# Performance work log

Hardware: AMD Instinct MI355X
Metric: run time of the kernel (lower is better)

The kernel has to match this reference:

```python
import jax, jax.numpy as jnp
import numpy as np

N_NODES = 100000


def _gcn_conv(h, row, col, norm, W, b):
    # h: [N, Fin] -> [N, Fout]; standard GCN: scatter-add of normalized
    # neighbor messages after linear transform.
    h = h @ W                                   # [N, Fout]
    msg = h[col] * norm[:, None]                # [E, Fout] gather + scale
    out = jax.ops.segment_sum(msg, row, num_segments=N_NODES)
    return out + b


def setup_inputs() -> dict:
    key = jax.random.key(0)
    k1, k2, k3, k4 = jax.random.split(key, 4)
    N, E, F_IN, HID, OUT = N_NODES, 3200000, 512, 16, 40
    x = jax.random.normal(k1, (N, F_IN), dtype=jnp.float32)
    edge_index = jax.random.randint(k2, (2, E), 0, N, dtype=jnp.int64)
    W1 = jax.random.normal(k3, (F_IN, HID), dtype=jnp.float32) * (1.0 / np.sqrt(F_IN))
    b1 = jnp.zeros((HID,), dtype=jnp.float32)
    W2 = jax.random.normal(k4, (HID, OUT), dtype=jnp.float32) * (1.0 / np.sqrt(HID))
    b2 = jnp.zeros((OUT,), dtype=jnp.float32)
    return {"x": x, "edge_index": edge_index, "W1": W1, "b1": b1, "W2": W2, "b2": b2}


def reference(x, edge_index, W1, b1, W2, b2):
    N = N_NODES
    # add self-loops (GCN convention)
    loop = jnp.arange(N, dtype=edge_index.dtype)
    row = jnp.concatenate([edge_index[0], loop])  # target nodes
    col = jnp.concatenate([edge_index[1], loop])  # source nodes
    # symmetric normalization deg^-1/2 * deg^-1/2
    deg = jax.ops.segment_sum(jnp.ones_like(row, dtype=x.dtype), row, num_segments=N)
    dinv = jnp.where(deg > 0, jax.lax.rsqrt(deg), 0.0)
    norm = dinv[row] * dinv[col]                  # [E+N]

    h = _gcn_conv(x, row, col, norm, W1, b1)
    h = jax.nn.relu(h)
    out = _gcn_conv(h, row, col, norm, W2, b2)
    return out
```

## Files before the change

### kernel.cpp

```cpp
#include <hip/hip_runtime.h>

#define N_NODES 100000
#define F_IN 512
#define HID 16
#define F_OUT 40

#define NB 784
#define BSHIFT 7
#define ROWS_PB 128
#define BCAP 4608
#define CUR_PAD 16
#define APAD 17
#define PARTB 512
#define SROW 129

__global__ void k_zero(int* __restrict__ g) {
    int i = blockIdx.x * 256 + threadIdx.x;
    if (i < NB * CUR_PAD) g[i] = 0;
}

__global__ __launch_bounds__(512) void k_fat(const float* __restrict__ x,
                                             const float* __restrict__ W1,
                                             const int* __restrict__ ei, int E,
                                             int* __restrict__ gcursor,
                                             unsigned int* __restrict__ sortbuf,
                                             float* __restrict__ Hs) {
    __shared__ float smem[8 * 64 * APAD];
    int t = threadIdx.x;
    if (blockIdx.x < PARTB) {
        int* lcnt = (int*)smem;
        int* gb   = lcnt + NB;
        int epb = (E + PARTB - 1) / PARTB;
        int base = blockIdx.x * epb;
        int lim = min(base + epb, E);
        for (int cbase = base; cbase < lim; cbase += 4096) {
            int cend = min(cbase + 4096, lim);
            for (int i = t; i < NB; i += 512) lcnt[i] = 0;
            __syncthreads();
            unsigned int v[8]; int bkt[8], mi[8];
#pragma unroll
            for (int i = 0; i < 8; ++i) {
                int e = cbase + i * 512 + t;
                bkt[i] = -1;
                if (e < cend) {
                    int r = ei[e], c = ei[E + e];
                    bkt[i] = r >> BSHIFT;
                    v[i] = ((unsigned)(r & (ROWS_PB - 1)) << 17) | (unsigned)c;
                    mi[i] = atomicAdd(&lcnt[bkt[i]], 1);
                }
            }
            __syncthreads();
            for (int i = t; i < NB; i += 512)
                gb[i] = atomicAdd(&gcursor[i * CUR_PAD], lcnt[i]);
            __syncthreads();
#pragma unroll
            for (int i = 0; i < 8; ++i)
                if (bkt[i] >= 0) {
                    int idx = gb[bkt[i]] + mi[i];
                    if (idx < BCAP) sortbuf[(size_t)bkt[i] * BCAP + idx] = v[i];
                }
            __syncthreads();
        }
    } else {
        int bid = blockIdx.x - PARTB;
        int tilebase = bid * 64;
        int srow = t >> 5;
        int sseg = t & 31;
        int crow = t & 63;
        int ksub = __builtin_amdgcn_readfirstlane(t >> 6);

        float acc[HID];
#pragma unroll
        for (int f = 0; f < HID; ++f) acc[f] = 0.0f;

        float4 rg[4];
#pragma unroll
        for (int q = 0; q < 4; ++q) {
            int r = tilebase + q * 16 + srow;
            r = min(r, N_NODES - 1);
            rg[q] = *reinterpret_cast<const float4*>(x + (size_t)r * F_IN + sseg * 4);
        }
        for (int s = 0; s < 4; ++s) {
            __syncthreads();
#pragma unroll
            for (int q = 0; q < 4; ++q) {
                int base = (q * 16 + srow) * SROW + sseg * 4;
                smem[base + 0] = rg[q].x;
                smem[base + 1] = rg[q].y;
                smem[base + 2] = rg[q].z;
                smem[base + 3] = rg[q].w;
            }
            __syncthreads();
            if (s < 3) {
#pragma unroll
                for (int q = 0; q < 4; ++q) {
                    int r = tilebase + q * 16 + srow;
                    r = min(r, N_NODES - 1);
                    rg[q] = *reinterpret_cast<const float4*>(
                        x + (size_t)r * F_IN + (s + 1) * 128 + sseg * 4);
                }
            }
            const float* wp = W1 + (s * 128 + ksub * 16) * HID;
            int lbase = crow * SROW + ksub * 16;
#pragma unroll
            for (int kk = 0; kk < 16; ++kk) {
                float xv = smem[lbase + kk];
#pragma unroll
                for (int f = 0; f < HID; ++f)
                    acc[f] = fmaf(xv, wp[kk * HID + f], acc[f]);
            }
        }
        __syncthreads();
        int rbase = (ksub * 64 + crow) * APAD;
#pragma unroll
        for (int f = 0; f < HID; ++f) smem[rbase + f] = acc[f];
        __syncthreads();
#pragma unroll
        for (int p = 0; p < 2; ++p) {
            int o = p * 512 + t;
            int r = o >> 4, f = o & 15;
            int rgl = tilebase + r;
            if (rgl < N_NODES) {
                float sum = 0.0f;
#pragma unroll
                for (int c = 0; c < 8; ++c) sum += smem[(c * 64 + r) * APAD + f];
                Hs[(size_t)rgl * HID + f] = sum;
            }
        }
    }
}

__global__ __launch_bounds__(256) void k_build(const unsigned int* __restrict__ sortbuf,
                                               const int* __restrict__ gcursor,
                                               int* __restrict__ rowptr,
                                               float* __restrict__ dinv,
                                               int* __restrict__ colv,
                                               float* __restrict__ Hs) {
    __shared__ int bb[NB];
    __shared__ int s[256];
    __shared__ int hist[ROWS_PB];
    __shared__ int rstart[ROWS_PB];
    __shared__ int cur[ROWS_PB];
    __shared__ float sdinv[ROWS_PB];
    int b = blockIdx.x, t = threadIdx.x;

    int l0 = 0, l1 = 0, l2 = 0, l3 = 0;
    if (t < 196) {
        l0 = min(gcursor[(t * 4 + 0) * CUR_PAD], BCAP);
        l1 = min(gcursor[(t * 4 + 1) * CUR_PAD], BCAP);
        l2 = min(gcursor[(t * 4 + 2) * CUR_PAD], BCAP);
        l3 = min(gcursor[(t * 4 + 3) * CUR_PAD], BCAP);
    }
    int part = l0 + l1 + l2 + l3;
    s[t] = part;
    __syncthreads();
    for (int off = 1; off < 256; off <<= 1) {
        int a = (t >= off) ? s[t - off] : 0;
        __syncthreads();
        s[t] += a;
        __syncthreads();
    }
    if (t < 196) {
        int ex = s[t] - part;
        bb[t * 4 + 0] = ex;
        bb[t * 4 + 1] = ex + l0;
        bb[t * 4 + 2] = ex + l0 + l1;
        bb[t * 4 + 3] = ex + l0 + l1 + l2;
    }
    if (t < ROWS_PB) hist[t] = 0;
    __syncthreads();
    int gbase = bb[b];
    int n = min(gcursor[b * CUR_PAD], BCAP);
    if (b == 0 && t == 0) rowptr[N_NODES] = s[255];

    const unsigned int* sb = sortbuf + (size_t)b * BCAP;
    for (int i = t; i < n; i += 256) atomicAdd(&hist[sb[i] >> 17], 1);
    __syncthreads();
    int c0 = (t < ROWS_PB) ? hist[t] : 0;
    s[t] = c0;
    __syncthreads();
    for (int off = 1; off < 256; off <<= 1) {
        int a = (t >= off) ? s[t - off] : 0;
        __syncthreads();
        s[t] += a;
        __syncthreads();
    }
    if (t < ROWS_PB) {
        int ex = s[t] - c0;
        rstart[t] = ex;
        cur[t] = 0;
        float dv = rsqrtf((float)(c0 + 1));
        sdinv[t] = dv;
        int g = b * ROWS_PB + t;
        if (g < N_NODES) {
            rowptr[g] = gbase + ex;
            dinv[g] = dv;
        }
    }
    __syncthreads();
    for (int i = t; i < n; i += 256) {
        unsigned int v = sb[i];
        int lr = v >> 17;
        int pos = atomicAdd(&cur[lr], 1);
        colv[gbase + rstart[lr] + pos] = (int)(v & 0x1FFFFu);
    }
    __syncthreads();
    for (int i = t; i < ROWS_PB * 4; i += 256) {
        int row = i >> 2, q = i & 3;
        int g = b * ROWS_PB + row;
        if (g < N_NODES) {
            float4* p = reinterpret_cast<float4*>(Hs + (size_t)g * HID + q * 4);
            float4 vv = *p;
            float dv = sdinv[row];
            vv.x *= dv; vv.y *= dv; vv.z *= dv; vv.w *= dv;
            *p = vv;
        }
    }
}

__global__ __launch_bounds__(256) void k_agg1(const int* __restrict__ rowptr,
                                              const int* __restrict__ colv,
                                              const float* __restrict__ dinv,
                                              const float* __restrict__ Hs,
                                              const float* __restrict__ b1,
                                              float* __restrict__ h1s) {
    int wid = __builtin_amdgcn_readfirstlane((blockIdx.x * 256 + threadIdx.x) >> 6);
    if (wid >= N_NODES) return;
    int lane = threadIdx.x & 63;
    int f4 = lane & 3, sub = lane >> 2;
    int beg = rowptr[wid], end = rowptr[wid + 1];
    float dr = dinv[wid];
    float4 acc = make_float4(0.f, 0.f, 0.f, 0.f);
    for (int j = beg + sub; j < end; j += 16) {
        int c = colv[j];
        float4 hv = *reinterpret_cast<const float4*>(Hs + (size_t)c * HID + f4 * 4);
        acc.x += hv.x; acc.y += hv.y; acc.z += hv.z; acc.w += hv.w;
    }
#pragma unroll
    for (int d = 4; d < 64; d <<= 1) {
        acc.x += __shfl_xor(acc.x, d);
        acc.y += __shfl_xor(acc.y, d);
        acc.z += __shfl_xor(acc.z, d);
        acc.w += __shfl_xor(acc.w, d);
    }
    if (sub == 0) {
        float4 self = *reinterpret_cast<const float4*>(Hs + (size_t)wid * HID + f4 * 4);
        float4 bb = *reinterpret_cast<const float4*>(b1 + f4 * 4);
        float4 o;
        o.x = fmaxf((acc.x + self.x) * dr + bb.x, 0.f) * dr;
        o.y = fmaxf((acc.y + self.y) * dr + bb.y, 0.f) * dr;
        o.z = fmaxf((acc.z + self.z) * dr + bb.z, 0.f) * dr;
        o.w = fmaxf((acc.w + self.w) * dr + bb.w, 0.f) * dr;
        *reinterpret_cast<float4*>(h1s + (size_t)wid * HID + f4 * 4) = o;
    }
}

__global__ __launch_bounds__(256) void k_agg2(const int* __restrict__ rowptr,
                                              const int* __restrict__ colv,
                                              const float* __restrict__ dinv,
                                              const float* __restrict__ h1s,
                                              const float* __restrict__ W2,
                                              const float* __restrict__ b2,
                                              float* __restrict__ out) {
    int wid = __builtin_amdgcn_readfirstlane((blockIdx.x * 256 + threadIdx.x) >> 6);
    if (wid >= N_NODES) return;
    int lane = threadIdx.x & 63;
    int f4 = lane & 3, sub = lane >> 2;
    int beg = rowptr[wid], end = rowptr[wid + 1];
    float dr = dinv[wid];
    float4 acc = make_float4(0.f, 0.f, 0.f, 0.f);
    for (int j = beg + sub; j < end; j += 16) {
        int c = colv[j];
        float4 hv = *reinterpret_cast<const float4*>(h1s + (size_t)c * HID + f4 * 4);
        acc.x += hv.x; acc.y += hv.y; acc.z += hv.z; acc.w += hv.w;
    }
#pragma unroll
    for (int d = 4; d < 64; d <<= 1) {
        acc.x += __shfl_xor(acc.x, d);
        acc.y += __shfl_xor(acc.y, d);
        acc.z += __shfl_xor(acc.z, d);
        acc.w += __shfl_xor(acc.w, d);
    }
    float4 self = *reinterpret_cast<const float4*>(h1s + (size_t)wid * HID + f4 * 4);
    float4 w4;
    w4.x = (acc.x + self.x) * dr;
    w4.y = (acc.y + self.y) * dr;
    w4.z = (acc.z + self.z) * dr;
    w4.w = (acc.w + self.w) * dr;
    if (lane < F_OUT) {
        float o = b2[lane];
#pragma unroll
        for (int k = 0; k < HID; ++k) {
            float comp = (k & 3) == 0 ? w4.x : (k & 3) == 1 ? w4.y
                        : (k & 3) == 2 ? w4.z : w4.w;
            float wk = __shfl(comp, k >> 2);
            o = fmaf(wk, W2[k * F_OUT + lane], o);
        }
        out[(size_t)wid * F_OUT + lane] = o;
    }
}

extern "C" void kernel_launch(void* const* d_in, const int* in_sizes, int n_in,
                              void* d_out, int out_size, void* d_ws, size_t ws_size,
                              hipStream_t stream) {
    const float* x  = (const float*)d_in[0];
    const int* ei   = (const int*)d_in[1];
    const float* W1 = (const float*)d_in[2];
    const float* b1 = (const float*)d_in[3];
    const float* W2 = (const float*)d_in[4];
    const float* b2 = (const float*)d_in[5];
    float* out = (float*)d_out;
    const int E = in_sizes[1] / 2;

    int* gcursor          = (int*)d_ws;
    int* rowptr           = gcursor + 12544;
    float* dinv           = (float*)(rowptr + 100016);
    int* colv             = (int*)(dinv + 100032);
    unsigned int* sortbuf = (unsigned int*)(colv + 3200000);
    float* h1s            = (float*)sortbuf;
    float* Hs             = (float*)(sortbuf + 3612672);

    const int nbW = (N_NODES * 64 + 255) / 256;
    const int nbG = (N_NODES + 63) / 64;

    k_zero<<<(NB * CUR_PAD + 255) / 256, 256, 0, stream>>>(gcursor);
    k_fat<<<PARTB + nbG, 512, 0, stream>>>(x, W1, ei, E, gcursor, sortbuf, Hs);
    k_build<<<NB, 256, 0, stream>>>(sortbuf, gcursor, rowptr, dinv, colv, Hs);
    k_agg1<<<nbW, 256, 0, stream>>>(rowptr, colv, dinv, Hs, b1, h1s);
    k_agg2<<<nbW, 256, 0, stream>>>(rowptr, colv, dinv, h1s, W2, b2, out);
}
```

Measured before the change: 211.1 us.

## Split fused partition/GEMM kernel and partition each block's edges in one pass

The fused kernel that ran edge bucketing and the x@W1 GEMM in disjoint block ranges is split into two separate kernels launched back to back. The partition kernel now handles all of a block's edges (up to 13 per thread) in a single pass instead of a loop over 4096-edge chunks. It also splits the shared-memory histogram into two copies chosen by wavefront parity to reduce LDS atomic contention. This removes per-chunk global cursor atomics and barriers, but gives up the overlap of partition and GEMM inside one launch and adds a kernel boundary.

```diff
diff --git a/kernel.cpp b/kernel.cpp
--- a/kernel.cpp
+++ b/kernel.cpp
@@ -19,113 +19,110 @@
     if (i < NB * CUR_PAD) g[i] = 0;
 }
 
-__global__ __launch_bounds__(512) void k_fat(const float* __restrict__ x,
-                                             const float* __restrict__ W1,
-                                             const int* __restrict__ ei, int E,
-                                             int* __restrict__ gcursor,
-                                             unsigned int* __restrict__ sortbuf,
-                                             float* __restrict__ Hs) {
+__global__ __launch_bounds__(512) void k_part1(const int* __restrict__ ei, int E,
+                                               int* __restrict__ gcursor,
+                                               unsigned int* __restrict__ sortbuf) {
+    __shared__ int lcnt0[NB], lcnt1[NB], gb[NB];
+    int t = threadIdx.x;
+    int half = (t >> 6) & 1;
+    int* myl = half ? lcnt1 : lcnt0;
+    int epb = (E + PARTB - 1) / PARTB;
+    int base = blockIdx.x * epb;
+    int lim = min(base + epb, E);
+    for (int i = t; i < NB; i += 512) { lcnt0[i] = 0; lcnt1[i] = 0; }
+    __syncthreads();
+    unsigned int v[13]; int bkt[13], mi[13];
+#pragma unroll
+    for (int i = 0; i < 13; ++i) {
+        int e = base + i * 512 + t;
+        bkt[i] = -1;
+        if (e < lim) {
+            int r = ei[e], c = ei[E + e];
+            bkt[i] = r >> BSHIFT;
+            v[i] = ((unsigned)(r & (ROWS_PB - 1)) << 17) | (unsigned)c;
+            mi[i] = atomicAdd(&myl[bkt[i]], 1);
+        }
+    }
+    __syncthreads();
+    for (int i = t; i < NB; i += 512)
+        gb[i] = atomicAdd(&gcursor[i * CUR_PAD], lcnt0[i] + lcnt1[i]);
+    __syncthreads();
+#pragma unroll
+    for (int i = 0; i < 13; ++i)
+        if (bkt[i] >= 0) {
+            int slot = gb[bkt[i]] + (half ? lcnt0[bkt[i]] : 0) + mi[i];
+            if (slot < BCAP) sortbuf[(size_t)bkt[i] * BCAP + slot] = v[i];
+        }
+}
+
+__global__ __launch_bounds__(512) void k_gemm(const float* __restrict__ x,
+                                              const float* __restrict__ W1,
+                                              float* __restrict__ Hs) {
     __shared__ float smem[8 * 64 * APAD];
     int t = threadIdx.x;
-    if (blockIdx.x < PARTB) {
-        int* lcnt = (int*)smem;
-        int* gb   = lcnt + NB;
-        int epb = (E + PARTB - 1) / PARTB;
-        int base = blockIdx.x * epb;
-        int lim = min(base + epb, E);
-        for (int cbase = base; cbase < lim; cbase += 4096) {
-            int cend = min(cbase + 4096, lim);
-            for (int i = t; i < NB; i += 512) lcnt[i] = 0;
-            __syncthreads();
-            unsigned int v[8]; int bkt[8], mi[8];
-#pragma unroll
-            for (int i = 0; i < 8; ++i) {
-                int e = cbase + i * 512 + t;
-                bkt[i] = -1;
-                if (e < cend) {
-                    int r = ei[e], c = ei[E + e];
-                    bkt[i] = r >> BSHIFT;
-                    v[i] = ((unsigned)(r & (ROWS_PB - 1)) << 17) | (unsigned)c;
-                    mi[i] = atomicAdd(&lcnt[bkt[i]], 1);
-                }
+    int bid = blockIdx.x;
+    int tilebase = bid * 64;
+    int srow = t >> 5;
+    int sseg = t & 31;
+    int crow = t & 63;
+    int ksub = __builtin_amdgcn_readfirstlane(t >> 6);
+
+    float acc[HID];
+#pragma unroll
+    for (int f = 0; f < HID; ++f) acc[f] = 0.0f;
+
+    float4 rg[4];
+#pragma unroll
+    for (int q = 0; q < 4; ++q) {
+        int r = tilebase + q * 16 + srow;
+        r = min(r, N_NODES - 1);
+        rg[q] = *reinterpret_cast<const float4*>(x + (size_t)r * F_IN + sseg * 4);
+    }
+    for (int s = 0; s < 4; ++s) {
+        __syncthreads();
+#pragma unroll
+        for (int q = 0; q < 4; ++q) {
+            int base = (q * 16 + srow) * SROW + sseg * 4;
+            smem[base + 0] = rg[q].x;
+            smem[base + 1] = rg[q].y;
+            smem[base + 2] = rg[q].z;
+            smem[base + 3] = rg[q].w;
+        }
+        __syncthreads();
+        if (s < 3) {
+#pragma unroll
+            for (int q = 0; q < 4; ++q) {
+                int r = tilebase + q * 16 + srow;
+                r = min(r, N_NODES - 1);
+                rg[q] = *reinterpret_cast<const float4*>(
+                    x + (size_t)r * F_IN + (s + 1) * 128 + sseg * 4);
             }
-            __syncthreads();
-            for (int i = t; i < NB; i += 512)
-                gb[i] = atomicAdd(&gcursor[i * CUR_PAD], lcnt[i]);
-            __syncthreads();
-#pragma unroll
-            for (int i = 0; i < 8; ++i)
-                if (bkt[i] >= 0) {
-                    int idx = gb[bkt[i]] + mi[i];
-                    if (idx < BCAP) sortbuf[(size_t)bkt[i] * BCAP + idx] = v[i];
-                }
-            __syncthreads();
-        }
-    } else {
-        int bid = blockIdx.x - PARTB;
-        int tilebase = bid * 64;
-        int srow = t >> 5;
-        int sseg = t & 31;
-        int crow = t & 63;
-        int ksub = __builtin_amdgcn_readfirstlane(t >> 6);
-
-        float acc[HID];
-#pragma unroll
-        for (int f = 0; f < HID; ++f) acc[f] = 0.0f;
-
-        float4 rg[4];
-#pragma unroll
-        for (int q = 0; q < 4; ++q) {
-            int r = tilebase + q * 16 + srow;
-            r = min(r, N_NODES - 1);
-            rg[q] = *reinterpret_cast<const float4*>(x + (size_t)r * F_IN + sseg * 4);
-        }
-        for (int s = 0; s < 4; ++s) {
-            __syncthreads();
-#pragma unroll
-            for (int q = 0; q < 4; ++q) {
-                int base = (q * 16 + srow) * SROW + sseg * 4;
-                smem[base + 0] = rg[q].x;
-                smem[base + 1] = rg[q].y;
-                smem[base + 2] = rg[q].z;
-                smem[base + 3] = rg[q].w;
-            }
-            __syncthreads();
-            if (s < 3) {
-#pragma unroll
-                for (int q = 0; q < 4; ++q) {
-                    int r = tilebase + q * 16 + srow;
-                    r = min(r, N_NODES - 1);
-                    rg[q] = *reinterpret_cast<const float4*>(
-                        x + (size_t)r * F_IN + (s + 1) * 128 + sseg * 4);
-                }
-            }
-            const float* wp = W1 + (s * 128 + ksub * 16) * HID;
-            int lbase = crow * SROW + ksub * 16;
-#pragma unroll
-            for (int kk = 0; kk < 16; ++kk) {
-                float xv = smem[lbase + kk];
-#pragma unroll
-                for (int f = 0; f < HID; ++f)
-                    acc[f] = fmaf(xv, wp[kk * HID + f], acc[f]);
-            }
-        }
-        __syncthreads();
-        int rbase = (ksub * 64 + crow) * APAD;
-#pragma unroll
-        for (int f = 0; f < HID; ++f) smem[rbase + f] = acc[f];
-        __syncthreads();
-#pragma unroll
-        for (int p = 0; p < 2; ++p) {
-            int o = p * 512 + t;
-            int r = o >> 4, f = o & 15;
-            int rgl = tilebase + r;
-            if (rgl < N_NODES) {
-                float sum = 0.0f;
-#pragma unroll
-                for (int c = 0; c < 8; ++c) sum += smem[(c * 64 + r) * APAD + f];
-                Hs[(size_t)rgl * HID + f] = sum;
-            }
+        }
+        const float* wp = W1 + (s * 128 + ksub * 16) * HID;
+        int lbase = crow * SROW + ksub * 16;
+#pragma unroll
+        for (int kk = 0; kk < 16; ++kk) {
+            float xv = smem[lbase + kk];
+#pragma unroll
+            for (int f = 0; f < HID; ++f)
+                acc[f] = fmaf(xv, wp[kk * HID + f], acc[f]);
+        }
+    }
+    __syncthreads();
+    int rbase = (ksub * 64 + crow) * APAD;
+#pragma unroll
+    for (int f = 0; f < HID; ++f) smem[rbase + f] = acc[f];
+    __syncthreads();
+#pragma unroll
+    for (int p = 0; p < 2; ++p) {
+        int o = p * 512 + t;
+        int r = o >> 4, f = o & 15;
+        int rgl = tilebase + r;
+        if (rgl < N_NODES) {
+            float sum = 0.0f;
+#pragma unroll
+            for (int c = 0; c < 8; ++c) sum += smem[(c * 64 + r) * APAD + f];
+            Hs[(size_t)rgl * HID + f] = sum;
         }
     }
 }
@@ -324,7 +321,8 @@
     const int nbG = (N_NODES + 63) / 64;
 
     k_zero<<<(NB * CUR_PAD + 255) / 256, 256, 0, stream>>>(gcursor);
-    k_fat<<<PARTB + nbG, 512, 0, stream>>>(x, W1, ei, E, gcursor, sortbuf, Hs);
+    k_part1<<<PARTB, 512, 0, stream>>>(ei, E, gcursor, sortbuf);
+    k_gemm<<<nbG, 512, 0, stream>>>(x, W1, Hs);
     k_build<<<NB, 256, 0, stream>>>(sortbuf, gcursor, rowptr, dinv, colv, Hs);
     k_agg1<<<nbW, 256, 0, stream>>>(rowptr, colv, dinv, Hs, b1, h1s);
     k_agg2<<<nbW, 256, 0, stream>>>(rowptr, colv, dinv, h1s, W2, b2, out);
```

Result: slower. 217.7 us (+3.1%).
